# Performance work log

Hardware: AMD Instinct MI355X
Metric: run time of the kernel (lower is better)

## Reference

```python
import jax, jax.numpy as jnp
import numpy as np

N, E, G = 100000, 1600000, 128
IN, HID, HEADS, EDIM, OUT = 16, 32, 4, 8, 4
HC = HEADS * HID


def _p(k, shape):
    return jax.random.normal(k, shape, jnp.float32) * 0.1


def setup_inputs():
    key = jax.random.key(0)
    ks = list(jax.random.split(key, 24))
    nxt = iter(ks)
    d = dict(
        x=jax.random.normal(next(nxt), (N, IN), jnp.float32),
        edge_index=jax.random.randint(next(nxt), (2, E), 0, N),
        edge_attr=jax.random.normal(next(nxt), (E, EDIM), jnp.float32),
        batch=jnp.sort(jax.random.randint(next(nxt), (N,), 0, G)),
    )
    # conv1: in=IN -> heads*hid
    d['wl1'] = _p(next(nxt), (IN, HC));  d['bl1'] = jnp.zeros((HC,), jnp.float32)
    d['wr1'] = _p(next(nxt), (IN, HC));  d['br1'] = jnp.zeros((HC,), jnp.float32)
    d['we1'] = _p(next(nxt), (EDIM, HC)); d['att1'] = _p(next(nxt), (HEADS, HID)); d['bc1'] = jnp.zeros((HC,), jnp.float32)
    # conv2: in=HC -> heads*hid
    d['wl2'] = _p(next(nxt), (HC, HC));  d['bl2'] = jnp.zeros((HC,), jnp.float32)
    d['wr2'] = _p(next(nxt), (HC, HC));  d['br2'] = jnp.zeros((HC,), jnp.float32)
    d['we2'] = _p(next(nxt), (EDIM, HC)); d['att2'] = _p(next(nxt), (HEADS, HID)); d['bc2'] = jnp.zeros((HC,), jnp.float32)
    # conv3: in=HC -> 1*hid (heads=1)
    d['wl3'] = _p(next(nxt), (HC, HID)); d['bl3'] = jnp.zeros((HID,), jnp.float32)
    d['wr3'] = _p(next(nxt), (HC, HID)); d['br3'] = jnp.zeros((HID,), jnp.float32)
    d['we3'] = _p(next(nxt), (EDIM, HID)); d['att3'] = _p(next(nxt), (1, HID)); d['bc3'] = jnp.zeros((HID,), jnp.float32)
    d['w_fc1'] = _p(next(nxt), (HID, 2 * HID)); d['b_fc1'] = jnp.zeros((2 * HID,), jnp.float32)
    d['w_fc2'] = _p(next(nxt), (2 * HID, OUT)); d['b_fc2'] = jnp.zeros((OUT,), jnp.float32)
    return d


def _gatv2(x, src, dst, eattr, wl, bl, wr, br, we, att, bias, n):
    # PyG GATv2Conv: e_ij = a^T . leaky_relu(Wl x_j + Wr x_i + We e_ij)
    H, C = att.shape
    xl = (x @ wl + bl).reshape(-1, H, C)  # source transform [N,H,C]
    xr = (x @ wr + br).reshape(-1, H, C)  # target transform [N,H,C]
    ea = (eattr @ we).reshape(-1, H, C)   # edge transform   [E,H,C]
    e = jax.nn.leaky_relu(xl[src] + xr[dst] + ea, 0.2)  # [E,H,C]
    logit = jnp.einsum('ehc,hc->eh', e, att)            # [E,H]
    m = jax.ops.segment_max(logit, dst, num_segments=n)
    p = jnp.exp(logit - m[dst])
    s = jax.ops.segment_sum(p, dst, num_segments=n)
    alpha = p / (s[dst] + 1e-16)                        # segment softmax per dst
    out = jax.ops.segment_sum(xl[src] * alpha[:, :, None], dst, num_segments=n)
    return out.reshape(n, H * C) + bias


def reference(x, edge_index, edge_attr, batch,
              wl1, bl1, wr1, br1, we1, att1, bc1,
              wl2, bl2, wr2, br2, we2, att2, bc2,
              wl3, bl3, wr3, br3, we3, att3, bc3,
              w_fc1, b_fc1, w_fc2, b_fc2):
    n = x.shape[0]
    src, dst = edge_index[0], edge_index[1]
    # add_self_loops=True with fill_value='mean' (mean of incoming edge_attr per node)
    ones_e = jnp.ones((src.shape[0],), x.dtype)
    cnt = jax.ops.segment_sum(ones_e, dst, num_segments=n)
    loop_attr = jax.ops.segment_sum(edge_attr, dst, num_segments=n) / jnp.maximum(cnt, 1.0)[:, None]
    ar = jnp.arange(n)
    src_a = jnp.concatenate([src, ar])
    dst_a = jnp.concatenate([dst, ar])
    ea = jnp.concatenate([edge_attr, loop_attr], axis=0)

    h = jax.nn.elu(_gatv2(x, src_a, dst_a, ea, wl1, bl1, wr1, br1, we1, att1, bc1, n))
    h = jax.nn.elu(_gatv2(h, src_a, dst_a, ea, wl2, bl2, wr2, br2, we2, att2, bc2, n))
    h = jax.nn.elu(_gatv2(h, src_a, dst_a, ea, wl3, bl3, wr3, br3, we3, att3, bc3, n))

    # global mean pool over graphs
    gs = jax.ops.segment_sum(h, batch, num_segments=G)
    gc = jax.ops.segment_sum(jnp.ones((n,), h.dtype), batch, num_segments=G)
    g = gs / jnp.maximum(gc, 1.0)[:, None]

    g = jax.nn.elu(g @ w_fc1 + b_fc1)
    return g @ w_fc2 + b_fc2
```

## Files before the change

### kernel.cpp

```cpp
#include <hip/hip_runtime.h>
#include <cstdint>
#include <type_traits>

constexpr int GNUM = 128;

typedef _Float16 h2 __attribute__((ext_vector_type(2)));
typedef _Float16 h4 __attribute__((ext_vector_type(4)));
typedef _Float16 h8 __attribute__((ext_vector_type(8)));
typedef float f4 __attribute__((ext_vector_type(4)));


__global__ __launch_bounds__(256) void hist_kernel(const int* __restrict__ dst,
                                                   int* __restrict__ cnt, int E) {
  int i = blockIdx.x * 256 + threadIdx.x;
  if (i < E) atomicAdd(&cnt[dst[i]], 1);
}

__global__ __launch_bounds__(256) void scan_part_kernel(const int* __restrict__ cnt,
                                                        int* __restrict__ bpart, int n) {
  __shared__ int red[256];
  int base = blockIdx.x * 512;
  int t = threadIdx.x;
  int s = 0;
  int i0 = base + t, i1 = base + 256 + t;
  if (i0 < n) s += cnt[i0] + 1;
  if (i1 < n) s += cnt[i1] + 1;
  red[t] = s;
  __syncthreads();
  for (int off = 128; off > 0; off >>= 1) {
    if (t < off) red[t] += red[t + off];
    __syncthreads();
  }
  if (t == 0) bpart[blockIdx.x] = red[0];
}

__global__ __launch_bounds__(1024) void scan_top_kernel(const int* __restrict__ bpart,
                                                        int* __restrict__ boff,
                                                        int* __restrict__ row_ptr,
                                                        const int* __restrict__ batch,
                                                        int* __restrict__ gstart,
                                                        int B, int n) {
  __shared__ int buf[1024];
  int t = threadIdx.x;
  buf[t] = (t < B) ? bpart[t] : 0;
  __syncthreads();
  for (int off = 1; off < 1024; off <<= 1) {
    int v = (t >= off) ? buf[t - off] : 0;
    __syncthreads();
    buf[t] += v;
    __syncthreads();
  }
  if (t < B) boff[t] = (t == 0) ? 0 : buf[t - 1];
  if (t == 0) row_ptr[n] = buf[1023];
  if (t <= GNUM) {
    int lo = 0, hi = n;
    while (lo < hi) {
      int mid = (lo + hi) >> 1;
      if (batch[mid] < t) lo = mid + 1; else hi = mid;
    }
    gstart[t] = lo;
  }
}

__global__ __launch_bounds__(256) void scan_write_kernel(const int* __restrict__ cnt,
                                                         const int* __restrict__ boff,
                                                         int* __restrict__ row_ptr,
                                                         int* __restrict__ fill, int n) {
  __shared__ int red[256];
  int base = blockIdx.x * 512;
  int t = threadIdx.x;
  int i0 = base + 2 * t, i1 = base + 2 * t + 1;
  int v0 = (i0 < n) ? cnt[i0] + 1 : 0;
  int v1 = (i1 < n) ? cnt[i1] + 1 : 0;
  int val = v0 + v1;
  red[t] = val;
  __syncthreads();
  for (int off = 1; off < 256; off <<= 1) {
    int u = (t >= off) ? red[t - off] : 0;
    __syncthreads();
    red[t] += u;
    __syncthreads();
  }
  int o = boff[blockIdx.x] + red[t] - val;
  if (i0 < n) { row_ptr[i0] = o; fill[i0] = o; }
  if (i1 < n) { row_ptr[i1] = o + v0; fill[i1] = o + v0; }
}

__global__ __launch_bounds__(256) void scatter_kernel(const int* __restrict__ src,
                                                      const int* __restrict__ dst,
                                                      const float* __restrict__ ea,
                                                      int* __restrict__ fill,
                                                      int* __restrict__ csr_src,
                                                      _Float16* __restrict__ ea_csr, int E) {
  int i = blockIdx.x * 256 + threadIdx.x;
  if (i >= E) return;
  int d = dst[i];
  int p = atomicAdd(&fill[d], 1);
  csr_src[p] = src[i];
  float4 e0 = *(const float4*)&ea[(size_t)i * 8];
  float4 e1 = *(const float4*)&ea[(size_t)i * 8 + 4];
  h8 v;
  v[0] = (_Float16)e0.x; v[1] = (_Float16)e0.y; v[2] = (_Float16)e0.z; v[3] = (_Float16)e0.w;
  v[4] = (_Float16)e1.x; v[5] = (_Float16)e1.y; v[6] = (_Float16)e1.z; v[7] = (_Float16)e1.w;
  *(h8*)&ea_csr[(size_t)p * 8] = v;
}

__global__ __launch_bounds__(256) void selfloop_kernel(const int* __restrict__ row_ptr,
                                                       int* __restrict__ csr_src,
                                                       _Float16* __restrict__ ea_csr, int n) {
  int idx = blockIdx.x * 256 + threadIdx.x;
  int i = idx >> 3, c = idx & 7;
  if (i >= n) return;
  int s = row_ptr[i], e = row_ptr[i + 1] - 1;
  float a = 0.f;
  for (int j = s; j < e; j++) a += (float)ea_csr[(size_t)j * 8 + c];
  float inv = 1.f / fmaxf((float)(e - s), 1.f);
  ea_csr[(size_t)e * 8 + c] = (_Float16)(a * inv);
  if (c == 0) csr_src[e] = i;
}

__global__ __launch_bounds__(256) void pack_all_kernel(
    const float* __restrict__ wl1, _Float16* __restrict__ p1l,
    const float* __restrict__ wr1, _Float16* __restrict__ p1r,
    const float* __restrict__ wl2, _Float16* __restrict__ p2l,
    const float* __restrict__ wr2, _Float16* __restrict__ p2r,
    const float* __restrict__ wl3, _Float16* __restrict__ p3l,
    const float* __restrict__ wr3, _Float16* __restrict__ p3r) {
  int y = blockIdx.y;
  const float* w; _Float16* wp; int Kreal, Kpad, NC;
  switch (y) {
    case 0: w = wl1; wp = p1l; Kreal = 16;  Kpad = 32;  NC = 128; break;
    case 1: w = wr1; wp = p1r; Kreal = 16;  Kpad = 32;  NC = 128; break;
    case 2: w = wl2; wp = p2l; Kreal = 128; Kpad = 128; NC = 128; break;
    case 3: w = wr2; wp = p2r; Kreal = 128; Kpad = 128; NC = 128; break;
    case 4: w = wl3; wp = p3l; Kreal = 128; Kpad = 128; NC = 32;  break;
    default: w = wr3; wp = p3r; Kreal = 128; Kpad = 128; NC = 32; break;
  }
  int KB = Kpad / 32;
  int total = (NC / 16) * KB * 64;
  int idx = blockIdx.x * 256 + threadIdx.x;
  if (idx >= total) return;
  int lane = idx & 63;
  int blk = idx >> 6;
  int nt = blk / KB, kb = blk % KB;
  int col = nt * 16 + (lane & 15);
  int krow = kb * 32 + (lane >> 4) * 8;
  h8 v;
#pragma unroll
  for (int j = 0; j < 8; j++)
    v[j] = (krow + j < Kreal) ? (_Float16)w[(size_t)(krow + j) * NC + col] : (_Float16)0.f;
  *(h8*)&wp[(size_t)idx * 8] = v;
}


template <int K, int NCOLS>
__global__ __launch_bounds__(256) void k1m_kernel(const _Float16* __restrict__ x,
                                                  const _Float16* __restrict__ wp0,
                                                  const float* __restrict__ b0,
                                                  _Float16* __restrict__ out0,
                                                  const _Float16* __restrict__ wp1,
                                                  const float* __restrict__ b1,
                                                  _Float16* __restrict__ out1, int n) {
  constexpr int NT = NCOLS / 16, KB = K / 32;
  const _Float16* wp = blockIdx.y ? wp1 : wp0;
  const float* b = blockIdx.y ? b1 : b0;
  _Float16* out = blockIdx.y ? out1 : out0;

  int tid = threadIdx.x;
  int wave = tid >> 6, lane = tid & 63;
  int m = lane & 15, quad = lane >> 4;
  int node0 = blockIdx.x * 64 + wave * 16;

  h8 afrag[KB];
  int anode = node0 + m;
  if (anode < n) {
#pragma unroll
    for (int kb = 0; kb < KB; kb++)
      afrag[kb] = *(const h8*)&x[(size_t)anode * K + kb * 32 + quad * 8];
  } else {
#pragma unroll
    for (int kb = 0; kb < KB; kb++) afrag[kb] = (h8)(_Float16)0.f;
  }

  f4 acc[NT] = {};
#pragma unroll
  for (int nt = 0; nt < NT; nt++) {
#pragma unroll
    for (int kb = 0; kb < KB; kb++) {
      h8 bfrag = *(const h8*)&wp[((size_t)(nt * KB + kb) * 64 + lane) * 8];
      acc[nt] = __builtin_amdgcn_mfma_f32_16x16x32_f16(afrag[kb], bfrag, acc[nt], 0, 0, 0);
    }
  }

#pragma unroll
  for (int nt = 0; nt < NT; nt++) {
#pragma unroll
    for (int r = 0; r < 4; r++) {
      int row = node0 + quad * 4 + r;
      if (row < n) {
        int col = nt * 16 + m;
        out[(size_t)row * NCOLS + col] = (_Float16)(acc[nt][r] + b[col]);
      }
    }
  }
}

template <int NCOLS>
__global__ __launch_bounds__(256) void k1m16_kernel(const float* __restrict__ x,
                                                    const _Float16* __restrict__ wp0,
                                                    const float* __restrict__ b0,
                                                    _Float16* __restrict__ out0,
                                                    const _Float16* __restrict__ wp1,
                                                    const float* __restrict__ b1,
                                                    _Float16* __restrict__ out1, int n) {
  constexpr int NT = NCOLS / 16;
  const _Float16* wp = blockIdx.y ? wp1 : wp0;
  const float* b = blockIdx.y ? b1 : b0;
  _Float16* out = blockIdx.y ? out1 : out0;

  int tid = threadIdx.x;
  int wave = tid >> 6, lane = tid & 63;
  int m = lane & 15, quad = lane >> 4;
  int node0 = blockIdx.x * 64 + wave * 16;

  int anode = node0 + m;
  h8 afrag = (h8)(_Float16)0.f;
  if (anode < n && quad < 2) {
    float4 v0 = *(const float4*)&x[(size_t)anode * 16 + quad * 8];
    float4 v1 = *(const float4*)&x[(size_t)anode * 16 + quad * 8 + 4];
    afrag[0] = (_Float16)v0.x; afrag[1] = (_Float16)v0.y;
    afrag[2] = (_Float16)v0.z; afrag[3] = (_Float16)v0.w;
    afrag[4] = (_Float16)v1.x; afrag[5] = (_Float16)v1.y;
    afrag[6] = (_Float16)v1.z; afrag[7] = (_Float16)v1.w;
  }

  f4 acc[NT] = {};
#pragma unroll
  for (int nt = 0; nt < NT; nt++) {
    h8 bfrag = *(const h8*)&wp[((size_t)nt * 64 + lane) * 8];
    acc[nt] = __builtin_amdgcn_mfma_f32_16x16x32_f16(afrag, bfrag, acc[nt], 0, 0, 0);
  }

#pragma unroll
  for (int nt = 0; nt < NT; nt++) {
#pragma unroll
    for (int r = 0; r < 4; r++) {
      int row = node0 + quad * 4 + r;
      if (row < n) {
        int col = nt * 16 + m;
        out[(size_t)row * NCOLS + col] = (_Float16)(acc[nt][r] + b[col]);
      }
    }
  }
}

template <int H>
__global__ __launch_bounds__(128) void k2_kernel(
    const _Float16* __restrict__ xl, const _Float16* __restrict__ xr,
    const int* __restrict__ row_ptr, const int* __restrict__ csr_src,
    const _Float16* __restrict__ ea_csr, const float* __restrict__ we,
    const float* __restrict__ att, const float* __restrict__ bc,
    _Float16* __restrict__ out, int n) {
  constexpr int HC = H * 32;
  constexpr int NL = HC / 4;
  constexpr int NPB = 128 / NL;

  int tid = threadIdx.x;
  int ln = tid / NL, q = tid % NL;
  int c0 = 4 * q;
  int node = blockIdx.x * NPB + ln;
  if (node >= n) return;

  h2 w2[8][2];
#pragma unroll
  for (int k = 0; k < 8; k++) {
    float4 v = *(const float4*)&we[k * HC + c0];
    w2[k][0] = h2{(_Float16)v.x, (_Float16)v.y};
    w2[k][1] = h2{(_Float16)v.z, (_Float16)v.w};
  }
  const float LOG2E = 1.44269504088896f;
  float4 av = *(const float4*)&att[c0];
  h2 a0 = h2{(_Float16)(av.x * LOG2E), (_Float16)(av.y * LOG2E)};
  h2 a1 = h2{(_Float16)(av.z * LOG2E), (_Float16)(av.w * LOG2E)};
  h4 xrh = *(const h4*)&xr[(size_t)node * HC + c0];
  h2 xr0 = h2{xrh[0], xrh[1]}, xr1 = h2{xrh[2], xrh[3]};
  const h2 p2 = h2{(_Float16)0.2f, (_Float16)0.2f};

  float acc[4] = {0.f, 0.f, 0.f, 0.f};
  float s = 0.f;

  int start = row_ptr[node], end = row_ptr[node + 1];
  int len = end - start;
  int pairs = (len + 1) >> 1;

  int j1 = (start + 1 < end) ? start + 1 : start;
  float m1 = (start + 1 < end) ? 1.f : 0.f;
  int s0 = csr_src[start], s1 = csr_src[j1];
  h8 e0 = *(const h8*)&ea_csr[(size_t)start * 8];
  h8 e1 = *(const h8*)&ea_csr[(size_t)j1 * 8];
  h4 x0 = *(const h4*)&xl[(size_t)s0 * HC + c0];
  h4 x1 = *(const h4*)&xl[(size_t)s1 * HC + c0];

#pragma unroll 2
  for (int p = 0; p < pairs; p++) {
    int jn = start + 2 * (p + 1);
    int k0 = (jn < end) ? jn : start;
    int k1 = (jn + 1 < end) ? jn + 1 : k0;
    float nm1 = (jn + 1 < end) ? 1.f : 0.f;
    int ns0 = csr_src[k0], ns1 = csr_src[k1];
    h8 ne0 = *(const h8*)&ea_csr[(size_t)k0 * 8];
    h8 ne1 = *(const h8*)&ea_csr[(size_t)k1 * 8];

    h2 t00 = h2{x0[0], x0[1]} + xr0;
    h2 t01 = h2{x0[2], x0[3]} + xr1;
    h2 t10 = h2{x1[0], x1[1]} + xr0;
    h2 t11 = h2{x1[2], x1[3]} + xr1;
#pragma unroll
    for (int k = 0; k < 8; k++) {
      h2 ev0 = h2{e0[k], e0[k]};
      h2 ev1 = h2{e1[k], e1[k]};
      t00 += ev0 * w2[k][0];
      t01 += ev0 * w2[k][1];
      t10 += ev1 * w2[k][0];
      t11 += ev1 * w2[k][1];
    }
    t00 = __builtin_elementwise_max(t00, t00 * p2);
    t01 = __builtin_elementwise_max(t01, t01 * p2);
    t10 = __builtin_elementwise_max(t10, t10 * p2);
    t11 = __builtin_elementwise_max(t11, t11 * p2);
    h2 pd0 = t00 * a0 + t01 * a1;
    h2 pd1 = t10 * a0 + t11 * a1;
    float part0 = (float)pd0[0] + (float)pd0[1];
    float part1 = (float)pd1[0] + (float)pd1[1];

    h4 nx0 = *(const h4*)&xl[(size_t)ns0 * HC + c0];
    h4 nx1 = *(const h4*)&xl[(size_t)ns1 * HC + c0];

    part0 += __shfl_xor(part0, 1, 64);
    part1 += __shfl_xor(part1, 1, 64);
    part0 += __shfl_xor(part0, 2, 64);
    part1 += __shfl_xor(part1, 2, 64);
    part0 += __shfl_xor(part0, 4, 64);
    part1 += __shfl_xor(part1, 4, 64);
    float pe0 = __builtin_amdgcn_exp2f(part0);
    float pe1 = __builtin_amdgcn_exp2f(part1) * m1;
    s += pe0 + pe1;
#pragma unroll
    for (int i = 0; i < 4; i++)
      acc[i] += pe0 * (float)x0[i] + pe1 * (float)x1[i];

    s0 = ns0; s1 = ns1; e0 = ne0; e1 = ne1; x0 = nx0; x1 = nx1; m1 = nm1;
  }

  float inv = 1.f / (s + 1e-16f);
  h4 o;
#pragma unroll
  for (int i = 0; i < 4; i++) {
    float v = acc[i] * inv + bc[c0 + i];
    o[i] = (_Float16)(v > 0.f ? v : (__expf(v) - 1.f));
  }
  *(h4*)&out[(size_t)node * HC + c0] = o;
}

__global__ __launch_bounds__(256) void poolfc_kernel(const _Float16* __restrict__ h,
                                                     const int* __restrict__ gstart,
                                                     const float* __restrict__ w1,
                                                     const float* __restrict__ b1,
                                                     const float* __restrict__ w2,
                                                     const float* __restrict__ b2,
                                                     float* __restrict__ out) {
  __shared__ float red[256];
  __shared__ float g[32];
  __shared__ float a1[64];
  int gi = blockIdx.x;
  int t = threadIdx.x;
  int s = gstart[gi], e = gstart[gi + 1];
  int c = t & 31, rg = t >> 5;
  float acc = 0.f;
  for (int i = s + rg; i < e; i += 8) acc += (float)h[(size_t)i * 32 + c];
  red[t] = acc;
  __syncthreads();
  if (t < 128) red[t] += red[t + 128];
  __syncthreads();
  if (t < 64) red[t] += red[t + 64];
  __syncthreads();
  if (t < 32) g[t] = (red[t] + red[t + 32]) / fmaxf((float)(e - s), 1.f);
  __syncthreads();
  if (t < 64) {
    float v = b1[t];
    for (int k = 0; k < 32; k++) v += g[k] * w1[k * 64 + t];
    a1[t] = v > 0.f ? v : (__expf(v) - 1.f);
  }
  __syncthreads();
  if (t < 4) {
    float o = b2[t];
    for (int k = 0; k < 64; k++) o += a1[k] * w2[k * 4 + t];
    out[gi * 4 + t] = o;
  }
}


extern "C" void kernel_launch(void* const* d_in, const int* in_sizes, int n_in,
                              void* d_out, int out_size, void* d_ws, size_t ws_size,
                              hipStream_t stream) {
  const float* x     = (const float*)d_in[0];
  const int*   ei    = (const int*)d_in[1];
  const float* eattr = (const float*)d_in[2];
  const int*   batch = (const int*)d_in[3];
  const float *wl1 = (const float*)d_in[4],  *bl1 = (const float*)d_in[5];
  const float *wr1 = (const float*)d_in[6],  *br1 = (const float*)d_in[7];
  const float *we1 = (const float*)d_in[8],  *at1 = (const float*)d_in[9];
  const float *bc1 = (const float*)d_in[10];
  const float *wl2 = (const float*)d_in[11], *bl2 = (const float*)d_in[12];
  const float *wr2 = (const float*)d_in[13], *br2 = (const float*)d_in[14];
  const float *we2 = (const float*)d_in[15], *at2 = (const float*)d_in[16];
  const float *bc2 = (const float*)d_in[17];
  const float *wl3 = (const float*)d_in[18], *bl3 = (const float*)d_in[19];
  const float *wr3 = (const float*)d_in[20], *br3 = (const float*)d_in[21];
  const float *we3 = (const float*)d_in[22], *at3 = (const float*)d_in[23];
  const float *bc3 = (const float*)d_in[24];
  const float *wf1 = (const float*)d_in[25], *bf1 = (const float*)d_in[26];
  const float *wf2 = (const float*)d_in[27], *bf2 = (const float*)d_in[28];

  int N = in_sizes[0] / 16;
  int E = in_sizes[1] / 2;
  const int* srcp = ei;
  const int* dstp = ei + E;
  int EA = E + N;
  int NB = (N + 511) / 512;

  char* wsb = (char*)d_ws;
  size_t off = 0;
  auto alloc = [&](size_t bytes) -> char* {
    char* p = wsb + off;
    off += (bytes + 255) & ~(size_t)255;
    return p;
  };
  int*       cnt     = (int*)alloc((size_t)N * 4);
  int*       row_ptr = (int*)alloc((size_t)(N + 1) * 4);
  int*       fill    = (int*)alloc((size_t)N * 4);
  int*       bpart   = (int*)alloc((size_t)1024 * 4);
  int*       boff    = (int*)alloc((size_t)1024 * 4);
  int*       csr_src = (int*)alloc((size_t)EA * 4);
  _Float16*  ea_csr  = (_Float16*)alloc((size_t)EA * 8 * 2);
  _Float16*  xl      = (_Float16*)alloc((size_t)N * 128 * 2);
  _Float16*  xr      = (_Float16*)alloc((size_t)N * 128 * 2);
  _Float16*  h16     = (_Float16*)alloc((size_t)N * 128 * 2);
  _Float16*  h3      = (_Float16*)alloc((size_t)N * 32 * 2);
  int*       gstart  = (int*)alloc((size_t)(GNUM + 1) * 4);
  _Float16*  wp1l    = (_Float16*)alloc((size_t)32 * 128 * 2);
  _Float16*  wp1r    = (_Float16*)alloc((size_t)32 * 128 * 2);
  _Float16*  wp2l    = (_Float16*)alloc((size_t)128 * 128 * 2);
  _Float16*  wp2r    = (_Float16*)alloc((size_t)128 * 128 * 2);
  _Float16*  wp3l    = (_Float16*)alloc((size_t)128 * 32 * 2);
  _Float16*  wp3r    = (_Float16*)alloc((size_t)128 * 32 * 2);

  hipMemsetAsync(cnt, 0, (size_t)N * 4, stream);

  hist_kernel<<<(E + 255) / 256, 256, 0, stream>>>(dstp, cnt, E);
  scan_part_kernel<<<NB, 256, 0, stream>>>(cnt, bpart, N);
  scan_top_kernel<<<1, 1024, 0, stream>>>(bpart, boff, row_ptr, batch, gstart, NB, N);
  scan_write_kernel<<<NB, 256, 0, stream>>>(cnt, boff, row_ptr, fill, N);
  scatter_kernel<<<(E + 255) / 256, 256, 0, stream>>>(srcp, dstp, eattr, fill, csr_src, ea_csr, E);
  selfloop_kernel<<<(N * 8 + 255) / 256, 256, 0, stream>>>(row_ptr, csr_src, ea_csr, N);
  pack_all_kernel<<<dim3(8, 6), 256, 0, stream>>>(wl1, wp1l, wr1, wp1r,
                                                  wl2, wp2l, wr2, wp2r,
                                                  wl3, wp3l, wr3, wp3r);

  k1m16_kernel<128><<<dim3((N + 63) / 64, 2), 256, 0, stream>>>(
      x, wp1l, bl1, xl, wp1r, br1, xr, N);
  k2_kernel<4><<<(N + 3) / 4, 128, 0, stream>>>(xl, xr, row_ptr, csr_src, ea_csr,
                                                we1, at1, bc1, h16, N);
  k1m_kernel<128, 128><<<dim3((N + 63) / 64, 2), 256, 0, stream>>>(
      h16, wp2l, bl2, xl, wp2r, br2, xr, N);
  k2_kernel<4><<<(N + 3) / 4, 128, 0, stream>>>(xl, xr, row_ptr, csr_src, ea_csr,
                                                we2, at2, bc2, h16, N);
  k1m_kernel<128, 32><<<dim3((N + 63) / 64, 2), 256, 0, stream>>>(
      h16, wp3l, bl3, xl, wp3r, br3, xr, N);
  k2_kernel<1><<<(N + 15) / 16, 128, 0, stream>>>(xl, xr, row_ptr, csr_src, ea_csr,
                                                  we3, at3, bc3, h3, N);

  poolfc_kernel<<<GNUM, 256, 0, stream>>>(h3, gstart, wf1, bf1, wf2, bf2, (float*)d_out);
}
```

Measured before the change: 684.6 us.

## Degree-sort nodes for aggregation and reduce attention logits in packed fp16

Builds a per-node degree histogram during the scan, then a permutation that groups nodes by in-degree, and has the aggregation kernels process nodes in that order. Nodes sharing a wavefront then have similar edge counts, so fewer lanes sit idle waiting on long neighbour loops. The attention-logit butterfly reduction now shuffles one packed fp16 pair per step instead of two floats. This halves the shuffle count at the cost of fp16 accumulation precision. Output writes become scattered, and there is an extra permute kernel plus an indirection load.

```diff
diff --git a/kernel.cpp b/kernel.cpp
--- a/kernel.cpp
+++ b/kernel.cpp
@@ -3,6 +3,7 @@
 #include <type_traits>
 
 constexpr int GNUM = 128;
+constexpr int DBINS = 64;
 
 typedef _Float16 h2 __attribute__((ext_vector_type(2)));
 typedef _Float16 h4 __attribute__((ext_vector_type(4)));
@@ -17,14 +18,18 @@
 }
 
 __global__ __launch_bounds__(256) void scan_part_kernel(const int* __restrict__ cnt,
-                                                        int* __restrict__ bpart, int n) {
+                                                        int* __restrict__ bpart,
+                                                        int* __restrict__ deghist, int n) {
   __shared__ int red[256];
+  __shared__ int dh[DBINS];
   int base = blockIdx.x * 512;
   int t = threadIdx.x;
+  if (t < DBINS) dh[t] = 0;
+  __syncthreads();
   int s = 0;
   int i0 = base + t, i1 = base + 256 + t;
-  if (i0 < n) s += cnt[i0] + 1;
-  if (i1 < n) s += cnt[i1] + 1;
+  if (i0 < n) { int c = cnt[i0] + 1; s += c; atomicAdd(&dh[c < DBINS - 1 ? c : DBINS - 1], 1); }
+  if (i1 < n) { int c = cnt[i1] + 1; s += c; atomicAdd(&dh[c < DBINS - 1 ? c : DBINS - 1], 1); }
   red[t] = s;
   __syncthreads();
   for (int off = 128; off > 0; off >>= 1) {
@@ -32,6 +37,7 @@
     __syncthreads();
   }
   if (t == 0) bpart[blockIdx.x] = red[0];
+  if (t < DBINS && dh[t] > 0) atomicAdd(&deghist[t], dh[t]);
 }
 
 __global__ __launch_bounds__(1024) void scan_top_kernel(const int* __restrict__ bpart,
@@ -39,8 +45,11 @@
                                                         int* __restrict__ row_ptr,
                                                         const int* __restrict__ batch,
                                                         int* __restrict__ gstart,
+                                                        const int* __restrict__ deghist,
+                                                        int* __restrict__ degbase,
                                                         int B, int n) {
   __shared__ int buf[1024];
+  __shared__ int dsc[DBINS];
   int t = threadIdx.x;
   buf[t] = (t < B) ? bpart[t] : 0;
   __syncthreads();
@@ -60,6 +69,16 @@
     }
     gstart[t] = lo;
   }
+  int myc = 0;
+  if (t < DBINS) { myc = deghist[t]; dsc[t] = myc; }
+  __syncthreads();
+  for (int off = 1; off < DBINS; off <<= 1) {
+    int v = (t >= off && t < DBINS) ? dsc[t - off] : 0;
+    __syncthreads();
+    if (t < DBINS) dsc[t] += v;
+    __syncthreads();
+  }
+  if (t < DBINS) degbase[t] = dsc[t] - myc;
 }
 
 __global__ __launch_bounds__(256) void scan_write_kernel(const int* __restrict__ cnt,
@@ -84,6 +103,27 @@
   int o = boff[blockIdx.x] + red[t] - val;
   if (i0 < n) { row_ptr[i0] = o; fill[i0] = o; }
   if (i1 < n) { row_ptr[i1] = o + v0; fill[i1] = o + v0; }
+}
+
+__global__ __launch_bounds__(256) void permute_kernel(const int* __restrict__ cnt,
+                                                      int* __restrict__ degbase,
+                                                      int* __restrict__ perm, int n) {
+  __shared__ int lcnt[DBINS];
+  __shared__ int lbase[DBINS];
+  int t = threadIdx.x;
+  if (t < DBINS) lcnt[t] = 0;
+  __syncthreads();
+  int i = blockIdx.x * 256 + t;
+  int bin = 0, lr = 0;
+  if (i < n) {
+    int c = cnt[i] + 1;
+    bin = c < DBINS - 1 ? c : DBINS - 1;
+    lr = atomicAdd(&lcnt[bin], 1);
+  }
+  __syncthreads();
+  if (t < DBINS && lcnt[t] > 0) lbase[t] = atomicAdd(&degbase[t], lcnt[t]);
+  __syncthreads();
+  if (i < n) perm[lbase[bin] + lr] = i;
 }
 
 __global__ __launch_bounds__(256) void scatter_kernel(const int* __restrict__ src,
@@ -258,9 +298,9 @@
 __global__ __launch_bounds__(128) void k2_kernel(
     const _Float16* __restrict__ xl, const _Float16* __restrict__ xr,
     const int* __restrict__ row_ptr, const int* __restrict__ csr_src,
-    const _Float16* __restrict__ ea_csr, const float* __restrict__ we,
-    const float* __restrict__ att, const float* __restrict__ bc,
-    _Float16* __restrict__ out, int n) {
+    const _Float16* __restrict__ ea_csr, const int* __restrict__ perm,
+    const float* __restrict__ we, const float* __restrict__ att,
+    const float* __restrict__ bc, _Float16* __restrict__ out, int n) {
   constexpr int HC = H * 32;
   constexpr int NL = HC / 4;
   constexpr int NPB = 128 / NL;
@@ -268,8 +308,9 @@
   int tid = threadIdx.x;
   int ln = tid / NL, q = tid % NL;
   int c0 = 4 * q;
-  int node = blockIdx.x * NPB + ln;
-  if (node >= n) return;
+  int nidx = blockIdx.x * NPB + ln;
+  if (nidx >= n) return;
+  int node = perm[nidx];
 
   h2 w2[8][2];
 #pragma unroll
@@ -330,20 +371,18 @@
     t11 = __builtin_elementwise_max(t11, t11 * p2);
     h2 pd0 = t00 * a0 + t01 * a1;
     h2 pd1 = t10 * a0 + t11 * a1;
-    float part0 = (float)pd0[0] + (float)pd0[1];
-    float part1 = (float)pd1[0] + (float)pd1[1];
+    h2 pp = h2{(_Float16)(pd0[0] + pd0[1]), (_Float16)(pd1[0] + pd1[1])};
 
     h4 nx0 = *(const h4*)&xl[(size_t)ns0 * HC + c0];
     h4 nx1 = *(const h4*)&xl[(size_t)ns1 * HC + c0];
 
-    part0 += __shfl_xor(part0, 1, 64);
-    part1 += __shfl_xor(part1, 1, 64);
-    part0 += __shfl_xor(part0, 2, 64);
-    part1 += __shfl_xor(part1, 2, 64);
-    part0 += __shfl_xor(part0, 4, 64);
-    part1 += __shfl_xor(part1, 4, 64);
-    float pe0 = __builtin_amdgcn_exp2f(part0);
-    float pe1 = __builtin_amdgcn_exp2f(part1) * m1;
+#pragma unroll
+    for (int mseg = 1; mseg <= 4; mseg <<= 1) {
+      int pv = __shfl_xor(__builtin_bit_cast(int, pp), mseg, 64);
+      pp += __builtin_bit_cast(h2, pv);
+    }
+    float pe0 = __builtin_amdgcn_exp2f((float)pp[0]);
+    float pe1 = __builtin_amdgcn_exp2f((float)pp[1]) * m1;
     s += pe0 + pe1;
 #pragma unroll
     for (int i = 0; i < 4; i++)
@@ -436,11 +475,14 @@
     off += (bytes + 255) & ~(size_t)255;
     return p;
   };
-  int*       cnt     = (int*)alloc((size_t)N * 4);
+  int*       cnt     = (int*)alloc((size_t)N * 4 + 2 * DBINS * 4);
+  int*       deghist = cnt + N;
+  int*       degbase = cnt + N + DBINS;
   int*       row_ptr = (int*)alloc((size_t)(N + 1) * 4);
   int*       fill    = (int*)alloc((size_t)N * 4);
   int*       bpart   = (int*)alloc((size_t)1024 * 4);
   int*       boff    = (int*)alloc((size_t)1024 * 4);
+  int*       perm    = (int*)alloc((size_t)N * 4);
   int*       csr_src = (int*)alloc((size_t)EA * 4);
   _Float16*  ea_csr  = (_Float16*)alloc((size_t)EA * 8 * 2);
   _Float16*  xl      = (_Float16*)alloc((size_t)N * 128 * 2);
@@ -455,12 +497,14 @@
   _Float16*  wp3l    = (_Float16*)alloc((size_t)128 * 32 * 2);
   _Float16*  wp3r    = (_Float16*)alloc((size_t)128 * 32 * 2);
 
-  hipMemsetAsync(cnt, 0, (size_t)N * 4, stream);
+  hipMemsetAsync(cnt, 0, (size_t)N * 4 + 2 * DBINS * 4, stream);
 
   hist_kernel<<<(E + 255) / 256, 256, 0, stream>>>(dstp, cnt, E);
-  scan_part_kernel<<<NB, 256, 0, stream>>>(cnt, bpart, N);
-  scan_top_kernel<<<1, 1024, 0, stream>>>(bpart, boff, row_ptr, batch, gstart, NB, N);
+  scan_part_kernel<<<NB, 256, 0, stream>>>(cnt, bpart, deghist, N);
+  scan_top_kernel<<<1, 1024, 0, stream>>>(bpart, boff, row_ptr, batch, gstart,
+                                          deghist, degbase, NB, N);
   scan_write_kernel<<<NB, 256, 0, stream>>>(cnt, boff, row_ptr, fill, N);
+  permute_kernel<<<(N + 255) / 256, 256, 0, stream>>>(cnt, degbase, perm, N);
   scatter_kernel<<<(E + 255) / 256, 256, 0, stream>>>(srcp, dstp, eattr, fill, csr_src, ea_csr, E);
   selfloop_kernel<<<(N * 8 + 255) / 256, 256, 0, stream>>>(row_ptr, csr_src, ea_csr, N);
   pack_all_kernel<<<dim3(8, 6), 256, 0, stream>>>(wl1, wp1l, wr1, wp1r,
@@ -470,15 +514,15 @@
   k1m16_kernel<128><<<dim3((N + 63) / 64, 2), 256, 0, stream>>>(
       x, wp1l, bl1, xl, wp1r, br1, xr, N);
   k2_kernel<4><<<(N + 3) / 4, 128, 0, stream>>>(xl, xr, row_ptr, csr_src, ea_csr,
-                                                we1, at1, bc1, h16, N);
+                                                perm, we1, at1, bc1, h16, N);
   k1m_kernel<128, 128><<<dim3((N + 63) / 64, 2), 256, 0, stream>>>(
       h16, wp2l, bl2, xl, wp2r, br2, xr, N);
   k2_kernel<4><<<(N + 3) / 4, 128, 0, stream>>>(xl, xr, row_ptr, csr_src, ea_csr,
-                                                we2, at2, bc2, h16, N);
+                                                perm, we2, at2, bc2, h16, N);
   k1m_kernel<128, 32><<<dim3((N + 63) / 64, 2), 256, 0, stream>>>(
       h16, wp3l, bl3, xl, wp3r, br3, xr, N);
   k2_kernel<1><<<(N + 15) / 16, 128, 0, stream>>>(xl, xr, row_ptr, csr_src, ea_csr,
-                                                  we3, at3, bc3, h3, N);
+                                                  perm, we3, at3, bc3, h3, N);
 
   poolfc_kernel<<<GNUM, 256, 0, stream>>>(h3, gstart, wf1, bf1, wf2, bf2, (float*)d_out);
 }
```

Result: slower. 702.0 us (+2.5%).
